# Optimization experiments

Hardware: AMD Instinct MI355X
Metric: run time of the kernel (lower is better)

## Reference

```python
import jax, jax.numpy as jnp
import numpy as np

N, E, IN_DIM, HID, HEADS = 50000, 400000, 128, 64, 4
NEG_SLOPE, LN_EPS = 0.2, 1e-5


def setup_inputs() -> dict:
    key = jax.random.key(0)
    ks = jax.random.split(key, 12)
    x = jax.random.normal(ks[0], (N, IN_DIM), dtype=jnp.float32)
    edge_index = jax.random.randint(ks[1], (2, E), 0, N, dtype=jnp.int64)
    s = 1.0 / np.sqrt(HID)
    return {
        "x": x,
        "edge_index": edge_index,
        "W_gcn": jax.random.normal(ks[2], (IN_DIM, HID), dtype=jnp.float32) / np.sqrt(IN_DIM),
        "b_gcn": jnp.zeros((HID,), dtype=jnp.float32),
        "W_gat": jax.random.normal(ks[3], (HID, HEADS * HID), dtype=jnp.float32) * s,
        "att_src": jax.random.normal(ks[4], (HEADS, HID), dtype=jnp.float32) * s,
        "att_dst": jax.random.normal(ks[5], (HEADS, HID), dtype=jnp.float32) * s,
        "b_gat": jnp.zeros((HID,), dtype=jnp.float32),
        "W_patch": jax.random.normal(ks[6], (HID, HID), dtype=jnp.float32) * s,
        "b_patch": jnp.zeros((HID,), dtype=jnp.float32),
        "gamma": jnp.ones((HID,), dtype=jnp.float32),
        "beta": jnp.zeros((HID,), dtype=jnp.float32),
    }


def _forward(x, edge_index, W_gcn, b_gcn, W_gat, att_src, att_dst, b_gat,
             W_patch, b_patch, gamma, beta):
    n = x.shape[0]
    loop = jnp.arange(n, dtype=edge_index.dtype)
    src = jnp.concatenate([edge_index[0], loop])  # self-loops appended (PyG default)
    dst = jnp.concatenate([edge_index[1], loop])

    # ---- GCNConv: symmetric degree normalization + scatter-add ----
    deg = jax.ops.segment_sum(jnp.ones_like(dst, dtype=jnp.float32), dst, num_segments=n)
    dinv = jnp.where(deg > 0, jax.lax.rsqrt(deg), 0.0)
    norm = dinv[src] * dinv[dst]  # [E+N]
    xw = x @ W_gcn  # [N,HID]
    h1 = jax.ops.segment_sum(xw[src] * norm[:, None], dst, num_segments=n) + b_gcn
    h1 = jax.nn.relu(h1)

    # ---- GATConv (heads=4, concat=False -> mean over heads) ----
    z = (h1 @ W_gat).reshape(n, HEADS, HID)  # [N,H,C]
    a_s = jnp.einsum('nhc,hc->nh', z, att_src)  # [N,H]
    a_d = jnp.einsum('nhc,hc->nh', z, att_dst)
    e = jax.nn.leaky_relu(a_s[src] + a_d[dst], negative_slope=NEG_SLOPE)  # [E+N,H]
    # segment-softmax over incoming edges per destination node
    m = jax.ops.segment_max(e, dst, num_segments=n)  # [N,H]
    ex = jnp.exp(e - m[dst])
    denom = jax.ops.segment_sum(ex, dst, num_segments=n)
    alpha = ex / denom[dst]  # [E+N,H]
    agg = jax.ops.segment_sum(z[src] * alpha[:, :, None], dst, num_segments=n)  # [N,H,C]
    h2 = jax.nn.relu(agg.mean(axis=1) + b_gat)

    # ---- residual fusion + LayerNorm (dropout is identity in eval) ----
    h_patch = h1 @ W_patch + b_patch
    h = h1 + h2 + h_patch
    mu = h.mean(axis=-1, keepdims=True)
    var = h.var(axis=-1, keepdims=True)
    return (h - mu) * jax.lax.rsqrt(var + LN_EPS) * gamma + beta


def reference(x, edge_index, W_gcn, b_gcn, W_gat, att_src, att_dst, b_gat,
              W_patch, b_patch, gamma, beta):
    return _forward(x, edge_index, W_gcn, b_gcn, W_gat, att_src, att_dst, b_gat,
                    W_patch, b_patch, gamma, beta)
```

## Files before the change

kernel.cpp:

```cpp
#include <hip/hip_runtime.h>
#include <math.h>

#define IN_DIM 128
#define HID 64
#define HEADS 4
#define NEG_SLOPE 0.2f
#define LN_EPS 1e-5f
#define APAD 328

typedef short bf16x8 __attribute__((ext_vector_type(8)));
typedef float f32x4  __attribute__((ext_vector_type(4)));
typedef unsigned short u16x4 __attribute__((ext_vector_type(4)));

__device__ inline unsigned short f2bf(float f) {
    unsigned u = __float_as_uint(f);
    u += 0x7fffu + ((u >> 16) & 1u);
    return (unsigned short)(u >> 16);
}
__device__ inline float bf2f(unsigned short s) {
    return __uint_as_float(((unsigned)s) << 16);
}
__device__ inline float leaky(float v) { return v > 0.0f ? v : NEG_SLOPE * v; }

__global__ void k_init_all(const unsigned long long* ei, int E, int n,
                           int* flag, int* hist,
                           const float* __restrict__ Wg, const float* __restrict__ Wp,
                           const float* __restrict__ Wgcn,
                           const float* __restrict__ att_s, const float* __restrict__ att_d,
                           unsigned short* __restrict__ Wt_post,
                           unsigned short* __restrict__ Wt_xw,
                           float* __restrict__ w_s, float* __restrict__ w_d) {
    int nzb = (n + 255) >> 8;
    int t = threadIdx.x;
    if ((int)blockIdx.x < nzb) {
        int i = blockIdx.x * 256 + t;
        if (i < n) hist[i] = 0;
        if (blockIdx.x == 0) {
            __shared__ int s_bad;
            if (t == 0) s_bad = 0;
            __syncthreads();
            int lim = E < 4096 ? E : 4096;
            int bad = 0;
            for (int k = t; k < lim; k += 256)
                if (ei[k] >= (unsigned long long)n) bad = 1;
            if (bad) s_bad = 1;
            __syncthreads();
            if (t == 0) *flag = s_bad ? 0 : 1;
        }
        return;
    }
    int role = blockIdx.x - nzb;
    if (role < 14) {
        int p = role * 256 + t;
        if (p < 2560) {
            int c = p & 63, kg = p >> 6;
            bf16x8 v;
#pragma unroll
            for (int j = 0; j < 8; j++) {
                int k = kg * 8 + j;
                float f;
                if (k < 256) f = 0.25f * Wg[(size_t)(k & 63) * 256 + (k >> 6) * 64 + c];
                else         f = Wp[(size_t)(k - 256) * 64 + c];
                v[j] = (short)f2bf(f);
            }
            *(bf16x8*)(&Wt_post[(size_t)p * 8]) = v;
        } else if (p < 2560 + 1024) {
            int q = p - 2560;
            int c = q & 63, kg = q >> 6;
            bf16x8 v;
#pragma unroll
            for (int j = 0; j < 8; j++)
                v[j] = (short)f2bf(Wgcn[(size_t)(kg * 8 + j) * 64 + c]);
            *(bf16x8*)(&Wt_xw[(size_t)q * 8]) = v;
        }
    } else {
        int h = t >> 6, k = t & 63;
        float ss = 0.0f, sd = 0.0f;
        for (int c = 0; c < HID; c++) {
            float w = Wg[(size_t)k * (HEADS * HID) + h * HID + c];
            ss += w * att_s[h * HID + c];
            sd += w * att_d[h * HID + c];
        }
        w_s[h * HID + k] = ss;
        w_d[h * HID + k] = sd;
    }
}

__global__ void k_hist(const void* ei, int E, const int* flag, int* hist) {
    int i = blockIdx.x * blockDim.x + threadIdx.x;
    if (i >= E) return;
    int is64 = *flag;
    int d;
    if (is64) d = (int)((const long long*)ei)[E + i];
    else      d = ((const int*)ei)[E + i];
    atomicAdd(&hist[d], 1);
}

__global__ __launch_bounds__(256) void k_scan1(const int* __restrict__ hist,
                                               int* __restrict__ tmp,
                                               int* __restrict__ partial, int n) {
    __shared__ int s[256];
    int t = threadIdx.x, i = blockIdx.x * 256 + t;
    int v = (i < n) ? hist[i] : 0;
    s[t] = v;
    __syncthreads();
    for (int off = 1; off < 256; off <<= 1) {
        int x = (t >= off) ? s[t - off] : 0;
        __syncthreads();
        s[t] += x;
        __syncthreads();
    }
    tmp[i] = s[t] - v;
    if (t == 255) partial[blockIdx.x] = s[255];
}

__global__ __launch_bounds__(256) void k_scan_apply(const int* __restrict__ tmp,
                                                    const int* __restrict__ partial,
                                                    const int* __restrict__ hist,
                                                    int* __restrict__ row_ptr,
                                                    int* __restrict__ cursor,
                                                    float* __restrict__ dinv,
                                                    int n, int nscan) {
    __shared__ int s[256];
    __shared__ int excl_s;
    int t = threadIdx.x;
    int v = (t < nscan) ? partial[t] : 0;
    s[t] = v;
    __syncthreads();
    for (int off = 1; off < 256; off <<= 1) {
        int x = (t >= off) ? s[t - off] : 0;
        __syncthreads();
        s[t] += x;
        __syncthreads();
    }
    if (t == 0) excl_s = (blockIdx.x == 0) ? 0 : s[blockIdx.x - 1];
    __syncthreads();
    int excl = excl_s;
    int i = blockIdx.x * 256 + t;
    if (i < n) {
        int v2 = tmp[i] + excl;
        row_ptr[i] = v2;
        cursor[i] = v2;
        dinv[i] = rsqrtf((float)(hist[i] + 1));
    }
}

__global__ __launch_bounds__(256) void k_scatter_xw(const void* ei, int E,
                                                    const int* __restrict__ flag,
                                                    int* __restrict__ cursor,
                                                    int* __restrict__ col,
                                                    const float* __restrict__ x,
                                                    const unsigned short* __restrict__ Wt_g,
                                                    const float* __restrict__ dinv,
                                                    unsigned short* __restrict__ xws, int n) {
    __shared__ unsigned short Wt[16 * 64 * 8];
    int nsb = (E + 255) >> 8;
    if ((int)blockIdx.x < nsb) {
        int i = blockIdx.x * 256 + threadIdx.x;
        if (i >= E) return;
        int is64 = *flag;
        int s, d;
        if (is64) { s = (int)((const long long*)ei)[i]; d = (int)((const long long*)ei)[E + i]; }
        else      { s = ((const int*)ei)[i];            d = ((const int*)ei)[E + i]; }
        int pos = atomicAdd(&cursor[d], 1);
        col[pos] = s;
    } else {
        int bx = blockIdx.x - nsb;
        int t = threadIdx.x;
        for (int idx = t; idx < 1024; idx += 256)
            *(bf16x8*)(&Wt[idx * 8]) = *(const bf16x8*)(&Wt_g[(size_t)idx * 8]);
        __syncthreads();
        int lane = t & 63;
        int li = lane & 15, quad = lane >> 4;
        int w = t >> 6;
        int r0 = bx * 64 + w * 16;
        int rload = r0 + li; if (rload > n - 1) rload = n - 1;
        f32x4 acc[4];
#pragma unroll
        for (int i = 0; i < 4; i++) acc[i] = (f32x4){0.f, 0.f, 0.f, 0.f};
        const float* xp = x + (size_t)rload * IN_DIM + quad * 8;
#pragma unroll
        for (int ks = 0; ks < 4; ks++) {
            float4 p0 = *(const float4*)(xp + ks * 32);
            float4 p1 = *(const float4*)(xp + ks * 32 + 4);
            bf16x8 a;
            a[0] = (short)f2bf(p0.x); a[1] = (short)f2bf(p0.y);
            a[2] = (short)f2bf(p0.z); a[3] = (short)f2bf(p0.w);
            a[4] = (short)f2bf(p1.x); a[5] = (short)f2bf(p1.y);
            a[6] = (short)f2bf(p1.z); a[7] = (short)f2bf(p1.w);
            int kg = ks * 4 + quad;
#pragma unroll
            for (int tt = 0; tt < 4; tt++) {
                bf16x8 bfr = *(const bf16x8*)(&Wt[((kg * 64) + tt * 16 + li) * 8]);
                acc[tt] = __builtin_amdgcn_mfma_f32_16x16x32_bf16(a, bfr, acc[tt], 0, 0, 0);
            }
        }
#pragma unroll
        for (int reg = 0; reg < 4; reg++) {
            int r = r0 + quad * 4 + reg;
            if (r >= n) continue;
            float dv = dinv[r];
#pragma unroll
            for (int tt = 0; tt < 4; tt++)
                xws[(size_t)r * HID + tt * 16 + li] = f2bf(acc[tt][reg] * dv);
        }
    }
}

__global__ __launch_bounds__(256) void k_gcn(const int* __restrict__ col,
                                             const int* __restrict__ row_ptr,
                                             const int* __restrict__ hist,
                                             const float* __restrict__ dinv,
                                             const unsigned short* __restrict__ xws,
                                             const float* __restrict__ b,
                                             const float* __restrict__ w_s,
                                             const float* __restrict__ w_d,
                                             unsigned short* __restrict__ h1b,
                                             float4* __restrict__ a_s,
                                             float4* __restrict__ a_d, int n) {
    int t = threadIdx.x;
    int w = t >> 6, lane = t & 63, q = lane >> 4, li = lane & 15;
    int d = blockIdx.x * 4 + w;
    if (d >= n) return;
    int start = row_ptr[d], cnt = hist[d];
    float a0, a1, a2, a3;
    {
        u16x4 sv = *(const u16x4*)(xws + (size_t)d * HID + li * 4);
        float z = (q == 0) ? 1.0f : 0.0f;
        a0 = z * bf2f(sv[0]); a1 = z * bf2f(sv[1]);
        a2 = z * bf2f(sv[2]); a3 = z * bf2f(sv[3]);
    }
    int k = q;
    int s = (k < cnt) ? col[start + k] : -1;
    while (s >= 0) {
        int k2 = k + 4;
        int s2 = (k2 < cnt) ? col[start + k2] : -1;
        u16x4 v = *(const u16x4*)(xws + (size_t)s * HID + li * 4);
        a0 += bf2f(v[0]); a1 += bf2f(v[1]); a2 += bf2f(v[2]); a3 += bf2f(v[3]);
        k = k2; s = s2;
    }
    a0 += __shfl_xor(a0, 16, 64); a1 += __shfl_xor(a1, 16, 64);
    a2 += __shfl_xor(a2, 16, 64); a3 += __shfl_xor(a3, 16, 64);
    a0 += __shfl_xor(a0, 32, 64); a1 += __shfl_xor(a1, 32, 64);
    a2 += __shfl_xor(a2, 32, 64); a3 += __shfl_xor(a3, 32, 64);
    float dv = dinv[d];
    float4 bv = *(const float4*)(b + li * 4);
    float h0 = fmaxf(a0 * dv + bv.x, 0.0f);
    float h1 = fmaxf(a1 * dv + bv.y, 0.0f);
    float h2 = fmaxf(a2 * dv + bv.z, 0.0f);
    float h3 = fmaxf(a3 * dv + bv.w, 0.0f);
    if (q == 0) {
        u16x4 o;
        o[0] = f2bf(h0); o[1] = f2bf(h1); o[2] = f2bf(h2); o[3] = f2bf(h3);
        *(u16x4*)(h1b + (size_t)d * HID + li * 4) = o;
    }
    float4 u;
    u = *(const float4*)(w_s + 0 * 64 + li * 4);
    float vs0 = h0 * u.x + h1 * u.y + h2 * u.z + h3 * u.w;
    u = *(const float4*)(w_s + 1 * 64 + li * 4);
    float vs1 = h0 * u.x + h1 * u.y + h2 * u.z + h3 * u.w;
    u = *(const float4*)(w_s + 2 * 64 + li * 4);
    float vs2 = h0 * u.x + h1 * u.y + h2 * u.z + h3 * u.w;
    u = *(const float4*)(w_s + 3 * 64 + li * 4);
    float vs3 = h0 * u.x + h1 * u.y + h2 * u.z + h3 * u.w;
    u = *(const float4*)(w_d + 0 * 64 + li * 4);
    float vd0 = h0 * u.x + h1 * u.y + h2 * u.z + h3 * u.w;
    u = *(const float4*)(w_d + 1 * 64 + li * 4);
    float vd1 = h0 * u.x + h1 * u.y + h2 * u.z + h3 * u.w;
    u = *(const float4*)(w_d + 2 * 64 + li * 4);
    float vd2 = h0 * u.x + h1 * u.y + h2 * u.z + h3 * u.w;
    u = *(const float4*)(w_d + 3 * 64 + li * 4);
    float vd3 = h0 * u.x + h1 * u.y + h2 * u.z + h3 * u.w;
#pragma unroll
    for (int o = 1; o <= 8; o <<= 1) {
        vs0 += __shfl_xor(vs0, o, 64); vs1 += __shfl_xor(vs1, o, 64);
        vs2 += __shfl_xor(vs2, o, 64); vs3 += __shfl_xor(vs3, o, 64);
        vd0 += __shfl_xor(vd0, o, 64); vd1 += __shfl_xor(vd1, o, 64);
        vd2 += __shfl_xor(vd2, o, 64); vd3 += __shfl_xor(vd3, o, 64);
    }
    if (lane == 0) {
        a_s[d] = make_float4(vs0, vs1, vs2, vs3);
        a_d[d] = make_float4(vd0, vd1, vd2, vd3);
    }
}

__global__ __launch_bounds__(256) void k_attn_post(
        const int* __restrict__ col, const int* __restrict__ row_ptr,
        const int* __restrict__ hist,
        const float4* __restrict__ a_s, const float4* __restrict__ a_d,
        const unsigned short* __restrict__ h1b,
        const unsigned short* __restrict__ Wt_g,
        const float* __restrict__ bp, const float* __restrict__ bg,
        const float* __restrict__ gamma, const float* __restrict__ beta,
        float* __restrict__ out, int n) {
    __shared__ unsigned short Atile[16 * APAD];
    __shared__ float hbuf[16 * 68];
    int t = threadIdx.x;
    int w = t >> 6, lane = t & 63, q = lane >> 4, li = lane & 15;
    int rowbase = blockIdx.x * 16;

    for (int j = 0; j < 4; j++) {
        int r = w * 4 + j;
        int d = rowbase + r;
        if (d >= n) {
            for (int c = lane; c < 320; c += 64) Atile[r * APAD + c] = 0;
            continue;
        }
        int start = row_ptr[d], cnt = hist[d];
        float4 ad = a_d[d];
        float4 asd = a_s[d];
        u16x4 sv = *(const u16x4*)(h1b + (size_t)d * HID + li * 4);
        float e0 = __expf(leaky(asd.x + ad.x));
        float e1 = __expf(leaky(asd.y + ad.y));
        float e2 = __expf(leaky(asd.z + ad.z));
        float e3 = __expf(leaky(asd.w + ad.w));
        float z = (q == 0) ? 1.0f : 0.0f;
        float f0 = bf2f(sv[0]), f1 = bf2f(sv[1]), f2 = bf2f(sv[2]), f3 = bf2f(sv[3]);
        f32x4 A0 = {z * e0 * f0, z * e0 * f1, z * e0 * f2, z * e0 * f3};
        f32x4 A1 = {z * e1 * f0, z * e1 * f1, z * e1 * f2, z * e1 * f3};
        f32x4 A2 = {z * e2 * f0, z * e2 * f1, z * e2 * f2, z * e2 * f3};
        f32x4 A3 = {z * e3 * f0, z * e3 * f1, z * e3 * f2, z * e3 * f3};
        float l0 = z * e0, l1 = z * e1, l2 = z * e2, l3 = z * e3;
        int k = q;
        int s = (k < cnt) ? col[start + k] : -1;
        while (s >= 0) {
            int k2 = k + 4;
            int s2 = (k2 < cnt) ? col[start + k2] : -1;
            float4 as = a_s[s];
            u16x4 hv = *(const u16x4*)(h1b + (size_t)s * HID + li * 4);
            float w0 = __expf(leaky(as.x + ad.x));
            float w1 = __expf(leaky(as.y + ad.y));
            float w2 = __expf(leaky(as.z + ad.z));
            float w3 = __expf(leaky(as.w + ad.w));
            float g0 = bf2f(hv[0]), g1 = bf2f(hv[1]);
            float g2 = bf2f(hv[2]), g3 = bf2f(hv[3]);
            A0[0] += w0 * g0; A0[1] += w0 * g1; A0[2] += w0 * g2; A0[3] += w0 * g3;
            A1[0] += w1 * g0; A1[1] += w1 * g1; A1[2] += w1 * g2; A1[3] += w1 * g3;
            A2[0] += w2 * g0; A2[1] += w2 * g1; A2[2] += w2 * g2; A2[3] += w2 * g3;
            A3[0] += w3 * g0; A3[1] += w3 * g1; A3[2] += w3 * g2; A3[3] += w3 * g3;
            l0 += w0; l1 += w1; l2 += w2; l3 += w3;
            k = k2; s = s2;
        }
#pragma unroll
        for (int c4 = 0; c4 < 4; c4++) {
            A0[c4] += __shfl_xor(A0[c4], 16, 64);
            A1[c4] += __shfl_xor(A1[c4], 16, 64);
            A2[c4] += __shfl_xor(A2[c4], 16, 64);
            A3[c4] += __shfl_xor(A3[c4], 16, 64);
        }
        l0 += __shfl_xor(l0, 16, 64); l1 += __shfl_xor(l1, 16, 64);
        l2 += __shfl_xor(l2, 16, 64); l3 += __shfl_xor(l3, 16, 64);
#pragma unroll
        for (int c4 = 0; c4 < 4; c4++) {
            A0[c4] += __shfl_xor(A0[c4], 32, 64);
            A1[c4] += __shfl_xor(A1[c4], 32, 64);
            A2[c4] += __shfl_xor(A2[c4], 32, 64);
            A3[c4] += __shfl_xor(A3[c4], 32, 64);
        }
        l0 += __shfl_xor(l0, 32, 64); l1 += __shfl_xor(l1, 32, 64);
        l2 += __shfl_xor(l2, 32, 64); l3 += __shfl_xor(l3, 32, 64);
        f32x4 Aq; float lq;
        if (q == 0)      { Aq = A0; lq = l0; }
        else if (q == 1) { Aq = A1; lq = l1; }
        else if (q == 2) { Aq = A2; lq = l2; }
        else             { Aq = A3; lq = l3; }
        float inv = 1.0f / lq;
        u16x4 o;
        o[0] = f2bf(Aq[0] * inv); o[1] = f2bf(Aq[1] * inv);
        o[2] = f2bf(Aq[2] * inv); o[3] = f2bf(Aq[3] * inv);
        *(u16x4*)(&Atile[r * APAD + q * 64 + li * 4]) = o;
        if (q == 0) *(u16x4*)(&Atile[r * APAD + 256 + li * 4]) = sv;
    }
    __syncthreads();

    f32x4 acc_a = {0.f, 0.f, 0.f, 0.f}, acc_h = {0.f, 0.f, 0.f, 0.f};
#pragma unroll
    for (int ks = 0; ks < 10; ks++) {
        int kg = ks * 4 + q;
        bf16x8 a = *(const bf16x8*)(&Atile[li * APAD + ks * 32 + q * 8]);
        bf16x8 bb = *(const bf16x8*)(&Wt_g[(size_t)(kg * 64 + w * 16 + li) * 8]);
        if (ks < 8) acc_a = __builtin_amdgcn_mfma_f32_16x16x32_bf16(a, bb, acc_a, 0, 0, 0);
        else        acc_h = __builtin_amdgcn_mfma_f32_16x16x32_bf16(a, bb, acc_h, 0, 0, 0);
    }
    int cc = w * 16 + li;
    float bgv = bg[cc], bpv = bp[cc];
#pragma unroll
    for (int reg = 0; reg < 4; reg++) {
        int r = q * 4 + reg;
        float h1c = bf2f(Atile[r * APAD + 256 + cc]);
        float h2v = fmaxf(acc_a[reg] + bgv, 0.0f);
        hbuf[r * 68 + cc] = h1c + h2v + acc_h[reg] + bpv;
    }
    __syncthreads();

    int row = t >> 4, lj = t & 15;
    f32x4 hv4 = *(const f32x4*)(&hbuf[row * 68 + lj * 4]);
    float s1 = (hv4[0] + hv4[1]) + (hv4[2] + hv4[3]);
    float s2 = (hv4[0] * hv4[0] + hv4[1] * hv4[1]) + (hv4[2] * hv4[2] + hv4[3] * hv4[3]);
#pragma unroll
    for (int o = 1; o <= 8; o <<= 1) {
        s1 += __shfl_xor(s1, o, 64);
        s2 += __shfl_xor(s2, o, 64);
    }
    float mu = s1 * (1.0f / 64.0f);
    float var = s2 * (1.0f / 64.0f) - mu * mu;
    float rs = rsqrtf(var + LN_EPS);
    int rg = rowbase + row;
    if (rg < n) {
        float4 g4 = *(const float4*)(gamma + lj * 4);
        float4 b4 = *(const float4*)(beta + lj * 4);
        float4 ov;
        ov.x = (hv4[0] - mu) * rs * g4.x + b4.x;
        ov.y = (hv4[1] - mu) * rs * g4.y + b4.y;
        ov.z = (hv4[2] - mu) * rs * g4.z + b4.z;
        ov.w = (hv4[3] - mu) * rs * g4.w + b4.w;
        *(float4*)(out + (size_t)rg * HID + lj * 4) = ov;
    }
}

extern "C" void kernel_launch(void* const* d_in, const int* in_sizes, int n_in,
                              void* d_out, int out_size, void* d_ws, size_t ws_size,
                              hipStream_t stream) {
    int n = in_sizes[0] / IN_DIM;
    int E = in_sizes[1] / 2;

    const float* x     = (const float*)d_in[0];
    const void*  ei    = d_in[1];
    const float* W_gcn = (const float*)d_in[2];
    const float* b_gcn = (const float*)d_in[3];
    const float* W_gat = (const float*)d_in[4];
    const float* att_s = (const float*)d_in[5];
    const float* att_d = (const float*)d_in[6];
    const float* b_gat = (const float*)d_in[7];
    const float* W_p   = (const float*)d_in[8];
    const float* b_p   = (const float*)d_in[9];
    const float* gamma = (const float*)d_in[10];
    const float* beta  = (const float*)d_in[11];

    int n_pad  = ((n + 255) / 256) * 256;
    int nscan  = n_pad / 256;
    int n128   = ((n + 127) / 128) * 128;
    int nzb    = (n + 255) / 256;
    int nsb    = (E + 255) / 256;

    float* ws = (float*)d_ws;
    size_t off = 0;
    int*   flag    = (int*)(ws + off);  off += 4;
    int*   hist    = (int*)(ws + off);  off += n;
    int*   row_ptr = (int*)(ws + off);  off += n;
    int*   cursor  = (int*)(ws + off);  off += n;
    int*   tmp     = (int*)(ws + off);  off += n_pad;
    int*   partial = (int*)(ws + off);  off += 256;
    int*   colv    = (int*)(ws + off);  off += E;
    float* dinv    = ws + off;          off += n;
    float* w_s     = ws + off;          off += HEADS * HID;
    float* w_d     = ws + off;          off += HEADS * HID;
    off = (off + 3) & ~(size_t)3;
    unsigned short* Wt_post = (unsigned short*)(ws + off); off += 2560 * 8 / 2;
    unsigned short* Wt_xw   = (unsigned short*)(ws + off); off += 1024 * 8 / 2;
    unsigned short* xws = (unsigned short*)(ws + off); off += (size_t)n * HID / 2;
    off = (off + 3) & ~(size_t)3;
    unsigned short* h1b = (unsigned short*)(ws + off); off += (size_t)n128 * HID / 2;
    off = (off + 3) & ~(size_t)3;
    float4* a_sv   = (float4*)(ws + off); off += (size_t)n * 4;
    float4* a_dv   = (float4*)(ws + off); off += (size_t)n * 4;

    k_init_all<<<nzb + 15, 256, 0, stream>>>((const unsigned long long*)ei, E, n,
                                             flag, hist, W_gat, W_p, W_gcn,
                                             att_s, att_d, Wt_post, Wt_xw, w_s, w_d);
    k_hist<<<nsb, 256, 0, stream>>>(ei, E, flag, hist);

    k_scan1<<<nscan, 256, 0, stream>>>(hist, tmp, partial, n);
    k_scan_apply<<<nscan, 256, 0, stream>>>(tmp, partial, hist, row_ptr, cursor,
                                            dinv, n, nscan);

    k_scatter_xw<<<nsb + (n + 63) / 64, 256, 0, stream>>>(ei, E, flag, cursor,
                                                          colv, x, Wt_xw,
                                                          dinv, xws, n);

    k_gcn<<<(n + 3) / 4, 256, 0, stream>>>(colv, row_ptr, hist, dinv, xws, b_gcn,
                                           w_s, w_d, h1b, a_sv, a_dv, n);

    k_attn_post<<<(n + 15) / 16, 256, 0, stream>>>(colv, row_ptr, hist, a_sv, a_dv,
                                                   h1b, Wt_post, b_p, b_gat,
                                                   gamma, beta, (float*)d_out, n);
}
```

Baseline: 214.9 us.

## Fuse front-end preprocessing kernels into one cooperative persistent kernel with grid syncs

Merges the init, histogram, two scan, and scatter/xw-GEMM kernels into a single cooperatively launched persistent kernel that separates phases with grid-wide barriers. It removes several kernel launches and the gaps between them. In exchange the grid is capped at the number of co-resident blocks, so the atomic histogram, scatter and GEMM phases now run as grid-stride loops, and each grid.sync adds its own barrier cost. The second-level scan over the block partials is also recomputed redundantly in every block.

```diff
diff --git a/kernel.cpp b/kernel.cpp
--- a/kernel.cpp
+++ b/kernel.cpp
@@ -1,5 +1,8 @@
 #include <hip/hip_runtime.h>
+#include <hip/hip_cooperative_groups.h>
 #include <math.h>
+
+namespace cg = cooperative_groups;
 
 #define IN_DIM 128
 #define HID 64
@@ -22,59 +25,50 @@
 }
 __device__ inline float leaky(float v) { return v > 0.0f ? v : NEG_SLOPE * v; }
 
-__global__ void k_init_all(const unsigned long long* ei, int E, int n,
-                           int* flag, int* hist,
-                           const float* __restrict__ Wg, const float* __restrict__ Wp,
-                           const float* __restrict__ Wgcn,
-                           const float* __restrict__ att_s, const float* __restrict__ att_d,
-                           unsigned short* __restrict__ Wt_post,
-                           unsigned short* __restrict__ Wt_xw,
-                           float* __restrict__ w_s, float* __restrict__ w_d) {
-    int nzb = (n + 255) >> 8;
+__global__ __launch_bounds__(256) void k_front(
+        const void* ei, int E, int n,
+        int* flag, int* hist, int* tmp, int* partial,
+        int* row_ptr, int* cursor, int* col, float* dinv,
+        const float* x,
+        const float* Wg, const float* Wp, const float* Wgcn,
+        const float* att_s, const float* att_d,
+        unsigned short* Wt_post, unsigned short* Wt_xw,
+        float* w_s, float* w_d,
+        unsigned short* xws) {
+    cg::grid_group grid = cg::this_grid();
+    __shared__ int s[256];
+    __shared__ int sp[256];
+    __shared__ int s_bad;
+    __shared__ unsigned short Wt[16 * 64 * 8];
     int t = threadIdx.x;
-    if ((int)blockIdx.x < nzb) {
-        int i = blockIdx.x * 256 + t;
-        if (i < n) hist[i] = 0;
-        if (blockIdx.x == 0) {
-            __shared__ int s_bad;
-            if (t == 0) s_bad = 0;
-            __syncthreads();
-            int lim = E < 4096 ? E : 4096;
-            int bad = 0;
-            for (int k = t; k < lim; k += 256)
-                if (ei[k] >= (unsigned long long)n) bad = 1;
-            if (bad) s_bad = 1;
-            __syncthreads();
-            if (t == 0) *flag = s_bad ? 0 : 1;
-        }
-        return;
-    }
-    int role = blockIdx.x - nzb;
-    if (role < 14) {
-        int p = role * 256 + t;
-        if (p < 2560) {
-            int c = p & 63, kg = p >> 6;
-            bf16x8 v;
-#pragma unroll
-            for (int j = 0; j < 8; j++) {
-                int k = kg * 8 + j;
-                float f;
-                if (k < 256) f = 0.25f * Wg[(size_t)(k & 63) * 256 + (k >> 6) * 64 + c];
-                else         f = Wp[(size_t)(k - 256) * 64 + c];
-                v[j] = (short)f2bf(f);
-            }
-            *(bf16x8*)(&Wt_post[(size_t)p * 8]) = v;
-        } else if (p < 2560 + 1024) {
-            int q = p - 2560;
-            int c = q & 63, kg = q >> 6;
-            bf16x8 v;
-#pragma unroll
-            for (int j = 0; j < 8; j++)
-                v[j] = (short)f2bf(Wgcn[(size_t)(kg * 8 + j) * 64 + c]);
-            *(bf16x8*)(&Wt_xw[(size_t)q * 8]) = v;
-        }
-    } else {
-        int h = t >> 6, k = t & 63;
+    int B = gridDim.x;
+    int T = B * 256;
+    int g = blockIdx.x * 256 + t;
+
+    for (int i = g; i < n; i += T) hist[i] = 0;
+    for (int p = g; p < 2560; p += T) {
+        int c = p & 63, kg = p >> 6;
+        bf16x8 v;
+#pragma unroll
+        for (int j = 0; j < 8; j++) {
+            int k = kg * 8 + j;
+            float f;
+            if (k < 256) f = 0.25f * Wg[(size_t)(k & 63) * 256 + (k >> 6) * 64 + c];
+            else         f = Wp[(size_t)(k - 256) * 64 + c];
+            v[j] = (short)f2bf(f);
+        }
+        *(bf16x8*)(&Wt_post[(size_t)p * 8]) = v;
+    }
+    for (int q = g; q < 1024; q += T) {
+        int c = q & 63, kg = q >> 6;
+        bf16x8 v;
+#pragma unroll
+        for (int j = 0; j < 8; j++)
+            v[j] = (short)f2bf(Wgcn[(size_t)(kg * 8 + j) * 64 + c]);
+        *(bf16x8*)(&Wt_xw[(size_t)q * 8]) = v;
+    }
+    for (int idx = g; idx < 256; idx += T) {
+        int h = idx >> 6, k = idx & 63;
         float ss = 0.0f, sd = 0.0f;
         for (int c = 0; c < HID; c++) {
             float w = Wg[(size_t)k * (HEADS * HID) + h * HID + c];
@@ -84,96 +78,87 @@
         w_s[h * HID + k] = ss;
         w_d[h * HID + k] = sd;
     }
-}
-
-__global__ void k_hist(const void* ei, int E, const int* flag, int* hist) {
-    int i = blockIdx.x * blockDim.x + threadIdx.x;
-    if (i >= E) return;
+    if (blockIdx.x == 0) {
+        if (t == 0) s_bad = 0;
+        __syncthreads();
+        int lim = E < 4096 ? E : 4096;
+        int bad = 0;
+        for (int k = t; k < lim; k += 256)
+            if (((const unsigned long long*)ei)[k] >= (unsigned long long)n) bad = 1;
+        if (bad) s_bad = 1;
+        __syncthreads();
+        if (t == 0) *flag = s_bad ? 0 : 1;
+    }
+    grid.sync();
+
     int is64 = *flag;
-    int d;
-    if (is64) d = (int)((const long long*)ei)[E + i];
-    else      d = ((const int*)ei)[E + i];
-    atomicAdd(&hist[d], 1);
-}
-
-__global__ __launch_bounds__(256) void k_scan1(const int* __restrict__ hist,
-                                               int* __restrict__ tmp,
-                                               int* __restrict__ partial, int n) {
-    __shared__ int s[256];
-    int t = threadIdx.x, i = blockIdx.x * 256 + t;
-    int v = (i < n) ? hist[i] : 0;
-    s[t] = v;
+    for (int i = g; i < E; i += T) {
+        int d;
+        if (is64) d = (int)((const long long*)ei)[E + i];
+        else      d = ((const int*)ei)[E + i];
+        atomicAdd(&hist[d], 1);
+    }
+    grid.sync();
+
+    int nch = (n + 255) >> 8;
+    for (int c = blockIdx.x; c < nch; c += B) {
+        int i = c * 256 + t;
+        int v = (i < n) ? hist[i] : 0;
+        s[t] = v;
+        __syncthreads();
+        for (int off = 1; off < 256; off <<= 1) {
+            int xv = (t >= off) ? s[t - off] : 0;
+            __syncthreads();
+            s[t] += xv;
+            __syncthreads();
+        }
+        tmp[i] = s[t] - v;
+        if (t == 255) partial[c] = s[255];
+        __syncthreads();
+    }
+    grid.sync();
+
+    {
+        int v = (t < nch) ? partial[t] : 0;
+        s[t] = v;
+        __syncthreads();
+        for (int off = 1; off < 256; off <<= 1) {
+            int xv = (t >= off) ? s[t - off] : 0;
+            __syncthreads();
+            s[t] += xv;
+            __syncthreads();
+        }
+        sp[t] = s[t];
+        __syncthreads();
+    }
+    for (int c = blockIdx.x; c < nch; c += B) {
+        int i = c * 256 + t;
+        if (i < n) {
+            int excl = (c == 0) ? 0 : sp[c - 1];
+            int v2 = tmp[i] + excl;
+            row_ptr[i] = v2;
+            cursor[i] = v2;
+            dinv[i] = rsqrtf((float)(hist[i] + 1));
+        }
+    }
+    grid.sync();
+
+    for (int i = g; i < E; i += T) {
+        int ss, dd;
+        if (is64) { ss = (int)((const long long*)ei)[i]; dd = (int)((const long long*)ei)[E + i]; }
+        else      { ss = ((const int*)ei)[i];            dd = ((const int*)ei)[E + i]; }
+        int pos = atomicAdd(&cursor[dd], 1);
+        col[pos] = ss;
+    }
+    for (int idx = t; idx < 1024; idx += 256)
+        *(bf16x8*)(&Wt[idx * 8]) = *(const bf16x8*)(&Wt_xw[(size_t)idx * 8]);
     __syncthreads();
-    for (int off = 1; off < 256; off <<= 1) {
-        int x = (t >= off) ? s[t - off] : 0;
-        __syncthreads();
-        s[t] += x;
-        __syncthreads();
-    }
-    tmp[i] = s[t] - v;
-    if (t == 255) partial[blockIdx.x] = s[255];
-}
-
-__global__ __launch_bounds__(256) void k_scan_apply(const int* __restrict__ tmp,
-                                                    const int* __restrict__ partial,
-                                                    const int* __restrict__ hist,
-                                                    int* __restrict__ row_ptr,
-                                                    int* __restrict__ cursor,
-                                                    float* __restrict__ dinv,
-                                                    int n, int nscan) {
-    __shared__ int s[256];
-    __shared__ int excl_s;
-    int t = threadIdx.x;
-    int v = (t < nscan) ? partial[t] : 0;
-    s[t] = v;
-    __syncthreads();
-    for (int off = 1; off < 256; off <<= 1) {
-        int x = (t >= off) ? s[t - off] : 0;
-        __syncthreads();
-        s[t] += x;
-        __syncthreads();
-    }
-    if (t == 0) excl_s = (blockIdx.x == 0) ? 0 : s[blockIdx.x - 1];
-    __syncthreads();
-    int excl = excl_s;
-    int i = blockIdx.x * 256 + t;
-    if (i < n) {
-        int v2 = tmp[i] + excl;
-        row_ptr[i] = v2;
-        cursor[i] = v2;
-        dinv[i] = rsqrtf((float)(hist[i] + 1));
-    }
-}
-
-__global__ __launch_bounds__(256) void k_scatter_xw(const void* ei, int E,
-                                                    const int* __restrict__ flag,
-                                                    int* __restrict__ cursor,
-                                                    int* __restrict__ col,
-                                                    const float* __restrict__ x,
-                                                    const unsigned short* __restrict__ Wt_g,
-                                                    const float* __restrict__ dinv,
-                                                    unsigned short* __restrict__ xws, int n) {
-    __shared__ unsigned short Wt[16 * 64 * 8];
-    int nsb = (E + 255) >> 8;
-    if ((int)blockIdx.x < nsb) {
-        int i = blockIdx.x * 256 + threadIdx.x;
-        if (i >= E) return;
-        int is64 = *flag;
-        int s, d;
-        if (is64) { s = (int)((const long long*)ei)[i]; d = (int)((const long long*)ei)[E + i]; }
-        else      { s = ((const int*)ei)[i];            d = ((const int*)ei)[E + i]; }
-        int pos = atomicAdd(&cursor[d], 1);
-        col[pos] = s;
-    } else {
-        int bx = blockIdx.x - nsb;
-        int t = threadIdx.x;
-        for (int idx = t; idx < 1024; idx += 256)
-            *(bf16x8*)(&Wt[idx * 8]) = *(const bf16x8*)(&Wt_g[(size_t)idx * 8]);
-        __syncthreads();
-        int lane = t & 63;
-        int li = lane & 15, quad = lane >> 4;
-        int w = t >> 6;
-        int r0 = bx * 64 + w * 16;
+    int lane = t & 63;
+    int li = lane & 15, quad = lane >> 4;
+    int wv = t >> 6;
+    int ntile = (n + 63) >> 6;
+    for (int bx = blockIdx.x; bx < ntile; bx += B) {
+        int r0 = bx * 64 + wv * 16;
         int rload = r0 + li; if (rload > n - 1) rload = n - 1;
         f32x4 acc[4];
 #pragma unroll
@@ -438,10 +423,7 @@
     const float* beta  = (const float*)d_in[11];
 
     int n_pad  = ((n + 255) / 256) * 256;
-    int nscan  = n_pad / 256;
     int n128   = ((n + 127) / 128) * 128;
-    int nzb    = (n + 255) / 256;
-    int nsb    = (E + 255) / 256;
 
     float* ws = (float*)d_ws;
     size_t off = 0;
@@ -465,18 +447,41 @@
     float4* a_sv   = (float4*)(ws + off); off += (size_t)n * 4;
     float4* a_dv   = (float4*)(ws + off); off += (size_t)n * 4;
 
-    k_init_all<<<nzb + 15, 256, 0, stream>>>((const unsigned long long*)ei, E, n,
-                                             flag, hist, W_gat, W_p, W_gcn,
-                                             att_s, att_d, Wt_post, Wt_xw, w_s, w_d);
-    k_hist<<<nsb, 256, 0, stream>>>(ei, E, flag, hist);
-
-    k_scan1<<<nscan, 256, 0, stream>>>(hist, tmp, partial, n);
-    k_scan_apply<<<nscan, 256, 0, stream>>>(tmp, partial, hist, row_ptr, cursor,
-                                            dinv, n, nscan);
-
-    k_scatter_xw<<<nsb + (n + 63) / 64, 256, 0, stream>>>(ei, E, flag, cursor,
-                                                          colv, x, Wt_xw,
-                                                          dinv, xws, n);
+    static int s_grid = 0;
+    if (s_grid == 0) {
+        int occ = 0;
+        hipOccupancyMaxActiveBlocksPerMultiprocessor(&occ, k_front, 256, 0);
+        if (occ < 1) occ = 1;
+        int sms = 0;
+        hipDeviceProp_t prop;
+        int dev = 0;
+        if (hipGetDevice(&dev) == hipSuccess &&
+            hipGetDeviceProperties(&prop, dev) == hipSuccess)
+            sms = prop.multiProcessorCount;
+        if (sms <= 0) sms = 256;
+        s_grid = occ * sms;
+    }
+    int grid = s_grid;
+    int needed = (E + 255) / 256;
+    if (grid > needed) grid = needed;
+    if (grid < 1) grid = 1;
+
+    const void* ei_a = ei; int E_a = E; int n_a = n;
+    const float* x_a = x;
+    const float* Wg_a = W_gat; const float* Wp_a = W_p; const float* Wgcn_a = W_gcn;
+    const float* as_a = att_s; const float* ad_a = att_d;
+    void* kargs[] = {
+        (void*)&ei_a, &E_a, &n_a,
+        &flag, &hist, &tmp, &partial,
+        &row_ptr, &cursor, &colv, &dinv,
+        (void*)&x_a,
+        (void*)&Wg_a, (void*)&Wp_a, (void*)&Wgcn_a,
+        (void*)&as_a, (void*)&ad_a,
+        &Wt_post, &Wt_xw,
+        &w_s, &w_d,
+        &xws
+    };
+    hipLaunchCooperativeKernel(k_front, dim3(grid), dim3(256), kargs, 0, stream);
 
     k_gcn<<<(n + 3) / 4, 256, 0, stream>>>(colv, row_ptr, hist, dinv, xws, b_gcn,
                                            w_s, w_d, h1b, a_sv, a_dv, n);
```

Result: slower. 450.5 us (+109.7%).

## Merge histogram into init and replace two-pass scan with decoupled lookback

Applied to the files above, without the earlier changes.

Clears the histogram with a memset and folds the edge-index format check and the destination histogram into the init kernel, each histogram block re-checking the format itself. The two-kernel prefix scan becomes a single-pass decoupled-lookback scan over per-chunk status words, cutting kernel launches and the intermediate tmp/partial buffers. The GCN kernel's attention-logit dot products are restructured so each 16-lane quarter computes one head instead of every lane computing all four, reducing shuffles. The lookback depends on blocks making forward progress and spins on global atomics, and the per-block format check adds redundant reads.

```diff
diff --git a/kernel.cpp b/kernel.cpp
--- a/kernel.cpp
+++ b/kernel.cpp
@@ -11,6 +11,7 @@
 typedef short bf16x8 __attribute__((ext_vector_type(8)));
 typedef float f32x4  __attribute__((ext_vector_type(4)));
 typedef unsigned short u16x4 __attribute__((ext_vector_type(4)));
+typedef unsigned long long ull;
 
 __device__ inline unsigned short f2bf(float f) {
     unsigned u = __float_as_uint(f);
@@ -22,34 +23,16 @@
 }
 __device__ inline float leaky(float v) { return v > 0.0f ? v : NEG_SLOPE * v; }
 
-__global__ void k_init_all(const unsigned long long* ei, int E, int n,
-                           int* flag, int* hist,
+__global__ __launch_bounds__(256) void k_init(const void* ei, int E, int n,
+                           int* flag, int* hist, ull* A,
                            const float* __restrict__ Wg, const float* __restrict__ Wp,
                            const float* __restrict__ Wgcn,
                            const float* __restrict__ att_s, const float* __restrict__ att_d,
                            unsigned short* __restrict__ Wt_post,
                            unsigned short* __restrict__ Wt_xw,
                            float* __restrict__ w_s, float* __restrict__ w_d) {
-    int nzb = (n + 255) >> 8;
     int t = threadIdx.x;
-    if ((int)blockIdx.x < nzb) {
-        int i = blockIdx.x * 256 + t;
-        if (i < n) hist[i] = 0;
-        if (blockIdx.x == 0) {
-            __shared__ int s_bad;
-            if (t == 0) s_bad = 0;
-            __syncthreads();
-            int lim = E < 4096 ? E : 4096;
-            int bad = 0;
-            for (int k = t; k < lim; k += 256)
-                if (ei[k] >= (unsigned long long)n) bad = 1;
-            if (bad) s_bad = 1;
-            __syncthreads();
-            if (t == 0) *flag = s_bad ? 0 : 1;
-        }
-        return;
-    }
-    int role = blockIdx.x - nzb;
+    int role = blockIdx.x;
     if (role < 14) {
         int p = role * 256 + t;
         if (p < 2560) {
@@ -73,7 +56,20 @@
                 v[j] = (short)f2bf(Wgcn[(size_t)(kg * 8 + j) * 64 + c]);
             *(bf16x8*)(&Wt_xw[(size_t)q * 8]) = v;
         }
-    } else {
+        return;
+    }
+    if (role == 14) {
+        A[t] = 0ULL;
+        __shared__ int s_bad;
+        if (t == 0) s_bad = 0;
+        __syncthreads();
+        int lim = E < 4096 ? E : 4096;
+        int bad = 0;
+        for (int k = t; k < lim; k += 256)
+            if (((const ull*)ei)[k] >= (ull)n) bad = 1;
+        if (bad) s_bad = 1;
+        __syncthreads();
+        if (t == 0) *flag = s_bad ? 0 : 1;
         int h = t >> 6, k = t & 63;
         float ss = 0.0f, sd = 0.0f;
         for (int c = 0; c < HID; c++) {
@@ -83,65 +79,86 @@
         }
         w_s[h * HID + k] = ss;
         w_d[h * HID + k] = sd;
-    }
-}
-
-__global__ void k_hist(const void* ei, int E, const int* flag, int* hist) {
-    int i = blockIdx.x * blockDim.x + threadIdx.x;
-    if (i >= E) return;
-    int is64 = *flag;
-    int d;
-    if (is64) d = (int)((const long long*)ei)[E + i];
-    else      d = ((const int*)ei)[E + i];
-    atomicAdd(&hist[d], 1);
-}
-
-__global__ __launch_bounds__(256) void k_scan1(const int* __restrict__ hist,
-                                               int* __restrict__ tmp,
-                                               int* __restrict__ partial, int n) {
+        return;
+    }
+    __shared__ int s_bad2;
+    if (t == 0) s_bad2 = 0;
+    __syncthreads();
+    int lim = E < 4096 ? E : 4096;
+    int bad = 0;
+    for (int k = t; k < lim; k += 256)
+        if (((const ull*)ei)[k] >= (ull)n) bad = 1;
+    if (bad) s_bad2 = 1;
+    __syncthreads();
+    int is64 = s_bad2 ? 0 : 1;
+    int hb = role - 15;
+    int nhb = gridDim.x - 15;
+    for (int i = hb * 256 + t; i < E; i += nhb * 256) {
+        int d;
+        if (is64) d = (int)((const long long*)ei)[E + i];
+        else      d = ((const int*)ei)[E + i];
+        atomicAdd(&hist[d], 1);
+    }
+}
+
+__global__ __launch_bounds__(256) void k_scan_lb(const int* __restrict__ hist,
+                                                 ull* __restrict__ A,
+                                                 int* __restrict__ row_ptr,
+                                                 int* __restrict__ cursor,
+                                                 float* __restrict__ dinv, int n) {
     __shared__ int s[256];
-    int t = threadIdx.x, i = blockIdx.x * 256 + t;
+    __shared__ int sbase;
+    int t = threadIdx.x, c = blockIdx.x;
+    int w = t >> 6, lane = t & 63;
+    int i = c * 256 + t;
     int v = (i < n) ? hist[i] : 0;
     s[t] = v;
     __syncthreads();
     for (int off = 1; off < 256; off <<= 1) {
-        int x = (t >= off) ? s[t - off] : 0;
+        int xv = (t >= off) ? s[t - off] : 0;
         __syncthreads();
-        s[t] += x;
+        s[t] += xv;
         __syncthreads();
     }
-    tmp[i] = s[t] - v;
-    if (t == 255) partial[blockIdx.x] = s[255];
-}
-
-__global__ __launch_bounds__(256) void k_scan_apply(const int* __restrict__ tmp,
-                                                    const int* __restrict__ partial,
-                                                    const int* __restrict__ hist,
-                                                    int* __restrict__ row_ptr,
-                                                    int* __restrict__ cursor,
-                                                    float* __restrict__ dinv,
-                                                    int n, int nscan) {
-    __shared__ int s[256];
-    __shared__ int excl_s;
-    int t = threadIdx.x;
-    int v = (t < nscan) ? partial[t] : 0;
-    s[t] = v;
-    __syncthreads();
-    for (int off = 1; off < 256; off <<= 1) {
-        int x = (t >= off) ? s[t - off] : 0;
-        __syncthreads();
-        s[t] += x;
-        __syncthreads();
-    }
-    if (t == 0) excl_s = (blockIdx.x == 0) ? 0 : s[blockIdx.x - 1];
-    __syncthreads();
-    int excl = excl_s;
-    int i = blockIdx.x * 256 + t;
+    int incl = s[t];
+    int S = s[255];
+    if (t == 0) {
+        if (c == 0) { sbase = 0; atomicExch(&A[0], (2ULL << 32) | (unsigned)S); }
+        else          atomicExch(&A[c], (1ULL << 32) | (unsigned)S);
+    }
+    if (c > 0 && w == 0) {
+        long long run = 0;
+        int p = c - 1;
+        for (;;) {
+            int idx = p - lane;
+            unsigned st, val;
+            if (idx >= 0) {
+                ull v2 = atomicAdd(&A[idx], 0ULL);
+                st = (unsigned)(v2 >> 32); val = (unsigned)v2;
+            } else { st = 2u; val = 0u; }
+            ull pm = __ballot(st == 2);
+            ull zm = __ballot(st == 0);
+            int firstP = pm ? (__ffsll((long long)pm) - 1) : 64;
+            int firstZ = zm ? (__ffsll((long long)zm) - 1) : 64;
+            if (firstZ < firstP) { __builtin_amdgcn_s_sleep(1); continue; }
+            unsigned contrib = (lane <= firstP) ? val : 0u;
+#pragma unroll
+            for (int o = 1; o <= 32; o <<= 1) contrib += __shfl_xor(contrib, o, 64);
+            run += contrib;
+            if (firstP < 64) break;
+            p -= 64;
+        }
+        if (lane == 0) {
+            sbase = (int)run;
+            atomicExch(&A[c], (2ULL << 32) | (unsigned)(run + (unsigned)S));
+        }
+    }
+    __syncthreads();
     if (i < n) {
-        int v2 = tmp[i] + excl;
-        row_ptr[i] = v2;
-        cursor[i] = v2;
-        dinv[i] = rsqrtf((float)(hist[i] + 1));
+        int excl = sbase + incl - v;
+        row_ptr[i] = excl;
+        cursor[i] = excl;
+        dinv[i] = rsqrtf((float)(v + 1));
     }
 }
 
@@ -254,33 +271,20 @@
         o[0] = f2bf(h0); o[1] = f2bf(h1); o[2] = f2bf(h2); o[3] = f2bf(h3);
         *(u16x4*)(h1b + (size_t)d * HID + li * 4) = o;
     }
-    float4 u;
-    u = *(const float4*)(w_s + 0 * 64 + li * 4);
-    float vs0 = h0 * u.x + h1 * u.y + h2 * u.z + h3 * u.w;
-    u = *(const float4*)(w_s + 1 * 64 + li * 4);
-    float vs1 = h0 * u.x + h1 * u.y + h2 * u.z + h3 * u.w;
-    u = *(const float4*)(w_s + 2 * 64 + li * 4);
-    float vs2 = h0 * u.x + h1 * u.y + h2 * u.z + h3 * u.w;
-    u = *(const float4*)(w_s + 3 * 64 + li * 4);
-    float vs3 = h0 * u.x + h1 * u.y + h2 * u.z + h3 * u.w;
-    u = *(const float4*)(w_d + 0 * 64 + li * 4);
-    float vd0 = h0 * u.x + h1 * u.y + h2 * u.z + h3 * u.w;
-    u = *(const float4*)(w_d + 1 * 64 + li * 4);
-    float vd1 = h0 * u.x + h1 * u.y + h2 * u.z + h3 * u.w;
-    u = *(const float4*)(w_d + 2 * 64 + li * 4);
-    float vd2 = h0 * u.x + h1 * u.y + h2 * u.z + h3 * u.w;
-    u = *(const float4*)(w_d + 3 * 64 + li * 4);
-    float vd3 = h0 * u.x + h1 * u.y + h2 * u.z + h3 * u.w;
+    float4 u  = *(const float4*)(w_s + q * 64 + li * 4);
+    float vs = h0 * u.x + h1 * u.y + h2 * u.z + h3 * u.w;
+    float4 u2 = *(const float4*)(w_d + q * 64 + li * 4);
+    float vd = h0 * u2.x + h1 * u2.y + h2 * u2.z + h3 * u2.w;
 #pragma unroll
     for (int o = 1; o <= 8; o <<= 1) {
-        vs0 += __shfl_xor(vs0, o, 64); vs1 += __shfl_xor(vs1, o, 64);
-        vs2 += __shfl_xor(vs2, o, 64); vs3 += __shfl_xor(vs3, o, 64);
-        vd0 += __shfl_xor(vd0, o, 64); vd1 += __shfl_xor(vd1, o, 64);
-        vd2 += __shfl_xor(vd2, o, 64); vd3 += __shfl_xor(vd3, o, 64);
-    }
+        vs += __shfl_xor(vs, o, 64);
+        vd += __shfl_xor(vd, o, 64);
+    }
+    float vs1 = __shfl(vs, 16, 64), vs2 = __shfl(vs, 32, 64), vs3 = __shfl(vs, 48, 64);
+    float vd1 = __shfl(vd, 16, 64), vd2 = __shfl(vd, 32, 64), vd3 = __shfl(vd, 48, 64);
     if (lane == 0) {
-        a_s[d] = make_float4(vs0, vs1, vs2, vs3);
-        a_d[d] = make_float4(vd0, vd1, vd2, vd3);
+        a_s[d] = make_float4(vs, vs1, vs2, vs3);
+        a_d[d] = make_float4(vd, vd1, vd2, vd3);
     }
 }
 
@@ -437,11 +441,11 @@
     const float* gamma = (const float*)d_in[10];
     const float* beta  = (const float*)d_in[11];
 
-    int n_pad  = ((n + 255) / 256) * 256;
-    int nscan  = n_pad / 256;
-    int n128   = ((n + 127) / 128) * 128;
-    int nzb    = (n + 255) / 256;
-    int nsb    = (E + 255) / 256;
+    int n128 = ((n + 127) / 128) * 128;
+    int nch  = (n + 255) / 256;
+    int nsb  = (E + 255) / 256;
+    int nhb  = nsb < 1024 ? nsb : 1024;
+    if (nhb < 1) nhb = 1;
 
     float* ws = (float*)d_ws;
     size_t off = 0;
@@ -449,12 +453,12 @@
     int*   hist    = (int*)(ws + off);  off += n;
     int*   row_ptr = (int*)(ws + off);  off += n;
     int*   cursor  = (int*)(ws + off);  off += n;
-    int*   tmp     = (int*)(ws + off);  off += n_pad;
-    int*   partial = (int*)(ws + off);  off += 256;
     int*   colv    = (int*)(ws + off);  off += E;
     float* dinv    = ws + off;          off += n;
     float* w_s     = ws + off;          off += HEADS * HID;
     float* w_d     = ws + off;          off += HEADS * HID;
+    off = (off + 1) & ~(size_t)1;
+    ull*   A       = (ull*)(ws + off);  off += 512;
     off = (off + 3) & ~(size_t)3;
     unsigned short* Wt_post = (unsigned short*)(ws + off); off += 2560 * 8 / 2;
     unsigned short* Wt_xw   = (unsigned short*)(ws + off); off += 1024 * 8 / 2;
@@ -465,14 +469,12 @@
     float4* a_sv   = (float4*)(ws + off); off += (size_t)n * 4;
     float4* a_dv   = (float4*)(ws + off); off += (size_t)n * 4;
 
-    k_init_all<<<nzb + 15, 256, 0, stream>>>((const unsigned long long*)ei, E, n,
-                                             flag, hist, W_gat, W_p, W_gcn,
-                                             att_s, att_d, Wt_post, Wt_xw, w_s, w_d);
-    k_hist<<<nsb, 256, 0, stream>>>(ei, E, flag, hist);
-
-    k_scan1<<<nscan, 256, 0, stream>>>(hist, tmp, partial, n);
-    k_scan_apply<<<nscan, 256, 0, stream>>>(tmp, partial, hist, row_ptr, cursor,
-                                            dinv, n, nscan);
+    hipMemsetAsync(hist, 0, (size_t)n * sizeof(int), stream);
+    k_init<<<15 + nhb, 256, 0, stream>>>(ei, E, n, flag, hist, A,
+                                         W_gat, W_p, W_gcn, att_s, att_d,
+                                         Wt_post, Wt_xw, w_s, w_d);
+
+    k_scan_lb<<<nch, 256, 0, stream>>>(hist, A, row_ptr, cursor, dinv, n);
 
     k_scatter_xw<<<nsb + (n + 63) / 64, 256, 0, stream>>>(ei, E, flag, cursor,
                                                           colv, x, Wt_xw,
```

Measured after the change: 209.1 us. -2.7%, faster.
